# Optimization experiments

Measured on AMD Instinct MI355X. Metric: run time of the kernel, lower is better.

## Reference

```python
import jax, jax.numpy as jnp
import numpy as np

# Static configuration matching the selected code path:
#   mode='inject_subject', is_self_attn=True, layer_id='up_blocks.0' (inject layer, bank hit)
#   alpha = AlphaScheduler.alpha(step=20, total=50, 'up_blocks.0') = 0.8 * 0.6 = 0.48
B, L, D, H = 4, 1024, 1280, 20
DH = D // H  # 64
ALPHA = 0.48


def setup_inputs() -> dict:
    key = jax.random.key(0)
    ks = jax.random.split(key, 8)
    w = lambda k, shp: (jax.random.normal(k, shp, dtype=jnp.float32) * 0.02)
    return {
        "hidden_states": jax.random.normal(ks[0], (B, L, D), dtype=jnp.float32),
        "Wq": w(ks[1], (D, D)),
        "Wk": w(ks[2], (D, D)),
        "Wv": w(ks[3], (D, D)),
        "Wo": w(ks[4], (D, D)),
        "bo": jnp.zeros((D,), dtype=jnp.float32),
        # cached background K/V, stored after head_to_batch_dim -> [B*H, L_bg, DH]
        "K_bg": jax.random.normal(ks[5], (B * H, L, DH), dtype=jnp.float32),
        "V_bg": jax.random.normal(ks[6], (B * H, L, DH), dtype=jnp.float32),
    }


def _head_to_batch(x):  # [B, L, D] -> [B*H, L, DH]
    b, l, _ = x.shape
    return x.reshape(b, l, H, DH).transpose(0, 2, 1, 3).reshape(b * H, l, DH)


def _batch_to_head(x):  # [B*H, L, DH] -> [B, L, D]
    bh, l, _ = x.shape
    b = bh // H
    return x.reshape(b, H, l, DH).transpose(0, 2, 1, 3).reshape(b, l, D)


def reference(hidden_states, Wq, Wk, Wv, Wo, bo, K_bg, V_bg):
    # q/k/v projections (self-attention: k, v from hidden_states)
    q = _head_to_batch(hidden_states @ Wq)  # [B*H, L, DH]
    k = _head_to_batch(hidden_states @ Wk)
    v = _head_to_batch(hidden_states @ Wv)

    # inject_subject: concat cached background K/V scaled by alpha along kv-seq dim
    k = jnp.concatenate([k, ALPHA * K_bg], axis=1)  # [B*H, 2L, DH]
    v = jnp.concatenate([v, ALPHA * V_bg], axis=1)

    # _sdpa: q scaled by scale*sqrt(dh), SDPA divides by sqrt(dh) -> net factor `scale`
    scale = 1.0 / jnp.sqrt(jnp.asarray(DH, dtype=q.dtype))
    scores = jnp.einsum('bqd,bkd->bqk', q, k) * scale  # [B*H, L, 2L]
    probs = jax.nn.softmax(scores, axis=-1)
    context = jnp.einsum('bqk,bkd->bqd', probs, v)  # [B*H, L, DH]

    out = _batch_to_head(context) @ Wo + bo  # to_out[0] linear
    return out
```

## Files before the change

kernel.cpp:

```cpp
#include <hip/hip_runtime.h>
#include <hip/hip_bf16.h>

#define B_   4
#define L_   1024
#define D_   1280
#define H_   20
#define DH_  64
#define BH_  (B_*H_)
#define L2_  (2*L_)
#define ALPHA_ 0.48f
#define QSCALE_ 0.180336880f

typedef __attribute__((ext_vector_type(8))) short short8;
typedef __attribute__((ext_vector_type(4))) float float4v;

__device__ __forceinline__ float exp2_fast(float x) {
    float r;
    asm volatile("v_exp_f32 %0, %1" : "=v"(r) : "v"(x));
    return r;
}

__device__ __forceinline__ ushort f2bf(float f) {
    union { float f; unsigned int i; } v; v.f = f;
    unsigned int i = v.i;
    unsigned int r = i + 0x7FFF + ((i >> 16) & 1);
    return (ushort)(r >> 16);
}
__device__ __forceinline__ short8 pack8(float4 f0, float4 f1) {
    short8 o;
    o[0] = (short)f2bf(f0.x); o[1] = (short)f2bf(f0.y);
    o[2] = (short)f2bf(f0.z); o[3] = (short)f2bf(f0.w);
    o[4] = (short)f2bf(f1.x); o[5] = (short)f2bf(f1.y);
    o[6] = (short)f2bf(f1.z); o[7] = (short)f2bf(f1.w);
    return o;
}
__device__ __forceinline__ void pack4_store(ushort* dst, float a, float b, float c, float d) {
    union { __hip_bfloat162 h; unsigned int u; } x, y;
    x.h = __float22bfloat162_rn(make_float2(a, b));
    y.h = __float22bfloat162_rn(make_float2(c, d));
    uint2 v; v.x = x.u; v.y = y.u;
    *(uint2*)dst = v;
}

__device__ __forceinline__ void async16(const void* g, void* l) {
    __builtin_amdgcn_global_load_lds(
        (__attribute__((address_space(1))) void*)g,
        (__attribute__((address_space(3))) void*)l, 16, 0, 0);
}

__global__ __launch_bounds__(256) void prep(
    const float* __restrict__ w0, const float* __restrict__ w1,
    const float* __restrict__ w2, const float* __restrict__ w3,
    ushort* __restrict__ Wt,
    const float* __restrict__ Vbg, ushort* __restrict__ Vt,
    const float* __restrict__ X, ushort* __restrict__ Xb,
    const float* __restrict__ Kbg, ushort* __restrict__ Kcv) {
    int bi = blockIdx.x, tid = threadIdx.x;
    __shared__ __align__(16) ushort t[64 * 72];
    if (bi < 2880) {
        bool doScale = (bi >= 1600);
        const float* src; int srcld; long sbase;
        ushort* dst = nullptr; int dstld = 0; long dbase = 0;
        ushort* vout = nullptr;
        if (bi < 1600) {
            int z = bi / 400, t4 = bi % 400;
            int by = t4 / 20, bx = t4 % 20;
            const float* srcs[4] = {w0, w1, w2, w3};
            src = srcs[z]; srcld = D_; dstld = D_;
            sbase = (long)(by * 64) * D_ + bx * 64;
            dst = Wt + (long)z * D_ * D_;
            dbase = (long)(bx * 64) * D_ + by * 64;
        } else {
            int j = bi - 1600;
            int bh = j >> 4, kt = j & 15;
            src = Vbg; srcld = DH_;
            sbase = ((long)bh * L_ + kt * 64) * DH_;
            vout = Vt + (((long)bh * 32 + 16 + kt) << 12);
        }
        int ldr = tid >> 3, ldc = (tid & 7) * 8;
#pragma unroll
        for (int i = 0; i < 2; i++) {
            int y = ldr + 32 * i;
            long idx = sbase + (long)y * srcld + ldc;
            float4 f0 = *(const float4*)&src[idx];
            float4 f1 = *(const float4*)&src[idx + 4];
            if (doScale) {
                f0.x *= ALPHA_; f0.y *= ALPHA_; f0.z *= ALPHA_; f0.w *= ALPHA_;
                f1.x *= ALPHA_; f1.y *= ALPHA_; f1.z *= ALPHA_; f1.w *= ALPHA_;
            }
            *(short8*)&t[y * 72 + ldc] = pack8(f0, f1);
        }
        __syncthreads();
        if (bi < 1600) {
            int r8 = (tid & 7) * 8, c0 = tid >> 3;
#pragma unroll
            for (int i = 0; i < 2; i++) {
                int c = c0 + i * 32;
                short8 o;
#pragma unroll
                for (int j2 = 0; j2 < 8; j2++) o[j2] = (short)t[(r8 + j2) * 72 + c];
                *(short8*)&dst[dbase + (long)c * dstld + r8] = o;
            }
        } else {
#pragma unroll
            for (int i = 0; i < 2; i++) {
                int jj = i * 256 + tid;
                int cc = jj >> 6, d2 = jj & 63;
                short8 o;
#pragma unroll
                for (int e = 0; e < 8; e++) o[e] = (short)t[(cc * 8 + e) * 72 + d2];
                *(short8*)&vout[(long)jj * 8] = o;
            }
        }
    } else if (bi < 5440) {
        long i = ((long)(bi - 2880) * 256 + tid) * 8;
        *(short8*)&Xb[i] = pack8(*(const float4*)&X[i], *(const float4*)&X[i + 4]);
    } else {
        int j2 = bi - 5440;
        int bh = j2 >> 4, kt = j2 & 15;
        const float* src = Kbg + ((long)bh * L_ + kt * 64) * DH_;
#pragma unroll
        for (int i = 0; i < 2; i++) {
            int r = i * 256 + tid;
            int kv = r >> 3, cd = r & 7;
            long idx = (long)kv * 64 + cd * 8;
            *(short8*)&t[kv * 72 + cd * 8] =
                pack8(*(const float4*)&src[idx], *(const float4*)&src[idx + 4]);
        }
        __syncthreads();
        ushort* outp = Kcv + (((long)bh * 16 + kt) << 12);
#pragma unroll
        for (int i = 0; i < 2; i++) {
            int jj = i * 256 + tid;
            int c = jj >> 6, kv = jj & 63;
            *(short8*)&outp[(long)jj * 8] = *(const short8*)&t[kv * 72 + c * 8];
        }
    }
}

template<int BMt, int BNt, int WROWS, int WCOLS>
__global__ __launch_bounds__(256) void gemm_tpl(
    const ushort* __restrict__ A, const ushort* __restrict__ Bt,
    ushort* __restrict__ Qp, ushort* __restrict__ Kp, ushort* __restrict__ Vt,
    float* __restrict__ Out, const float* __restrict__ bo, int mode) {
    constexpr int MI = BMt / WROWS / 16;
    constexpr int NI = BNt / WCOLS / 16;
    constexpr int ASZ = BMt * 32, BSZ = BNt * 32;
    constexpr int RB = 1280 / BNt;
    __shared__ __align__(16) ushort Al[2 * ASZ];
    __shared__ __align__(16) ushort Bl[2 * BSZ];
    int tid = threadIdx.x;
    int bx = blockIdx.x, by = blockIdx.y;
    int w = tid >> 6, lane = tid & 63, l15 = lane & 15, quad = lane >> 4;
    int wm = (w / WCOLS) * (BMt / WROWS);
    int wn = (w % WCOLS) * (BNt / WCOLS);
    float4v acc[MI][NI] = {};
    const int K = 1280;
    constexpr int NK = 40;
    const ushort* Arow = A + (long)by * BMt * K + (tid >> 2) * K + (tid & 3) * 8;
    const ushort* Brow = Bt + (long)bx * BNt * K + (tid >> 2) * K + (tid & 3) * 8;

    auto stage = [&](int ki, int b) {
#pragma unroll
        for (int i = 0; i < BMt / 64; i++)
            async16(Arow + (long)i * 64 * K + ki * 32, &Al[b * ASZ + (i * 4 + w) * 512]);
#pragma unroll
        for (int i = 0; i < BNt / 64; i++)
            async16(Brow + (long)i * 64 * K + ki * 32, &Bl[b * BSZ + (i * 4 + w) * 512]);
    };

    stage(0, 0);
    __syncthreads();
    for (int ki = 0; ki < NK; ki++) {
        int cur = ki & 1;
        if (ki + 1 < NK) stage(ki + 1, 1 - cur);
        short8 av[MI], bv[NI];
#pragma unroll
        for (int mi = 0; mi < MI; mi++)
            av[mi] = *(const short8*)&Al[cur * ASZ + (wm + mi * 16 + l15) * 32 + quad * 8];
#pragma unroll
        for (int ni = 0; ni < NI; ni++)
            bv[ni] = *(const short8*)&Bl[cur * BSZ + (wn + ni * 16 + l15) * 32 + quad * 8];
#pragma unroll
        for (int mi = 0; mi < MI; mi++)
#pragma unroll
            for (int ni = 0; ni < NI; ni++)
                acc[mi][ni] = __builtin_amdgcn_mfma_f32_16x16x32_bf16(av[mi], bv[ni], acc[mi][ni], 0, 0, 0);
        __syncthreads();
    }

    if (mode == 0) {
        int which = bx / RB;
#pragma unroll
        for (int mi = 0; mi < MI; mi++) {
            int m0 = by * BMt + wm + mi * 16 + quad * 4;
            int b = m0 >> 10, l0 = m0 & 1023;
#pragma unroll
            for (int ni = 0; ni < NI; ni++) {
                int n = bx * BNt + wn + ni * 16 + l15;
                int np = n - which * 1280;
                int h = np >> 6, dh = np & 63;
                if (which == 0) {
#pragma unroll
                    for (int r = 0; r < 4; r++)
                        Qp[((long)(b * H_ + h) * L_ + l0 + r) * DH_ + dh] =
                            f2bf(acc[mi][ni][r] * QSCALE_);
                } else if (which == 1) {
                    long kb = ((((long)(b * H_ + h) * 16 + (l0 >> 6)) * 8 + (dh >> 3)) * 64
                               + (l0 & 63)) * 8 + (dh & 7);
#pragma unroll
                    for (int r = 0; r < 4; r++)
                        Kp[kb + r * 8] = f2bf(acc[mi][ni][r]);
                } else {
                    pack4_store(&Vt[((((long)(b * H_ + h) * 32 + (l0 >> 6)) * 8
                                      + ((l0 & 63) >> 3)) * 64 + dh) * 8 + (l0 & 7)],
                                acc[mi][ni][0], acc[mi][ni][1],
                                acc[mi][ni][2], acc[mi][ni][3]);
                }
            }
        }
    } else {
#pragma unroll
        for (int mi = 0; mi < MI; mi++) {
            int mloc = wm + mi * 16 + quad * 4;
#pragma unroll
            for (int ni = 0; ni < NI; ni++) {
                int nloc = wn + ni * 16 + l15;
#pragma unroll
                for (int r = 0; r < 4; r++) {
                    int m = by * BMt + mloc + r;
                    int n = bx * BNt + nloc;
                    Out[(long)m * D_ + n] = acc[mi][ni][r] + bo[n];
                }
            }
        }
    }
}

#define FS 72

__global__ __launch_bounds__(256) void flash_attn(
    const ushort* __restrict__ Qp, const ushort* __restrict__ Kp,
    const ushort* __restrict__ Kbg, const ushort* __restrict__ Vt,
    ushort* __restrict__ Ctx) {
    __shared__ __align__(16) ushort Kl[2 * 4096], Vl[2 * 4096];
    __shared__ __align__(16) ushort Pl[128 * FS];
    int tid = threadIdx.x;
    int w = tid >> 6, lane = tid & 63, l15 = lane & 15, quad = lane >> 4;
    int bi = blockIdx.x;
    int bh = (bi & 7) * 10 + ((bi >> 3) % 10);
    int qt = bi / 80;

    short8 aq[2][2];
    const ushort* Qb = Qp + ((long)bh * L_ + qt * 128 + w * 32) * DH_;
#pragma unroll
    for (int mi = 0; mi < 2; mi++)
#pragma unroll
        for (int ks = 0; ks < 2; ks++)
            aq[mi][ks] = *(const short8*)&Qb[(mi * 16 + l15) * DH_ + ks * 32 + quad * 8];

    float rs[2] = {0.f, 0.f};
    float4v O[2][4] = {};
    int prow = (w * 32 + l15) * FS;

    auto stage = [&](int kt, int b) {
        const ushort* Ksrc = (kt < 16)
            ? Kp  + (((long)bh * 16 + kt) << 12)
            : Kbg + (((long)bh * 16 + (kt - 16)) << 12);
        const ushort* Vsrc = Vt + (((long)bh * 32 + kt) << 12);
#pragma unroll
        for (int i = 0; i < 2; i++) {
            int c = w * 2 + i;
            async16(&Ksrc[c * 512 + lane * 8], &Kl[b * 4096 + c * 512]);
            async16(&Vsrc[c * 512 + lane * 8], &Vl[b * 4096 + c * 512]);
        }
    };

    stage(0, 0);
    __syncthreads();
    for (int kt = 0; kt < 32; kt++) {
        int cur = kt & 1;
        if (kt + 1 < 32) stage(kt + 1, 1 - cur);
        bool bg = (kt >= 16);
        float4v s[4][2] = {};
#pragma unroll
        for (int ks = 0; ks < 2; ks++) {
            short8 bk[4];
#pragma unroll
            for (int nt = 0; nt < 4; nt++)
                bk[nt] = *(const short8*)&Kl[cur * 4096 + (ks * 4 + quad) * 512 + (nt * 16 + l15) * 8];
#pragma unroll
            for (int nt = 0; nt < 4; nt++)
#pragma unroll
                for (int mi = 0; mi < 2; mi++)
                    s[nt][mi] = __builtin_amdgcn_mfma_f32_16x16x32_bf16(bk[nt], aq[mi][ks], s[nt][mi], 0, 0, 0);
        }
#pragma unroll
        for (int nt = 0; nt < 4; nt++)
#pragma unroll
            for (int mi = 0; mi < 2; mi++) {
                float p[4];
#pragma unroll
                for (int r = 0; r < 4; r++) {
                    float sv = s[nt][mi][r];
                    if (bg) sv *= ALPHA_;
                    p[r] = exp2_fast(sv);
                    rs[mi] += p[r];
                }
                pack4_store(&Pl[prow + mi * 16 * FS + nt * 16 + quad * 4],
                            p[0], p[1], p[2], p[3]);
            }
        asm volatile("s_waitcnt lgkmcnt(0)" ::: "memory");
        __builtin_amdgcn_sched_barrier(0);
#pragma unroll
        for (int ks = 0; ks < 2; ks++) {
            short8 bv[4];
#pragma unroll
            for (int nt = 0; nt < 4; nt++)
                bv[nt] = *(const short8*)&Vl[cur * 4096 + (ks * 4 + quad) * 512 + (nt * 16 + l15) * 8];
            short8 ap[2];
#pragma unroll
            for (int mi = 0; mi < 2; mi++)
                ap[mi] = *(const short8*)&Pl[prow + mi * 16 * FS + ks * 32 + quad * 8];
#pragma unroll
            for (int nt = 0; nt < 4; nt++)
#pragma unroll
                for (int mi = 0; mi < 2; mi++)
                    O[mi][nt] = __builtin_amdgcn_mfma_f32_16x16x32_bf16(bv[nt], ap[mi], O[mi][nt], 0, 0, 0);
        }
        __syncthreads();
    }
    int b = bh / H_, h = bh % H_;
#pragma unroll
    for (int mi = 0; mi < 2; mi++) {
        float v = rs[mi];
        v += __shfl_xor(v, 16);
        v += __shfl_xor(v, 32);
        float rcp = 1.f / v;
        long l = qt * 128 + w * 32 + mi * 16 + l15;
#pragma unroll
        for (int nt = 0; nt < 4; nt++)
            pack4_store(&Ctx[(long)(b * L_ + l) * D_ + h * DH_ + nt * 16 + quad * 4],
                        O[mi][nt][0] * rcp, O[mi][nt][1] * rcp,
                        O[mi][nt][2] * rcp, O[mi][nt][3] * rcp);
    }
}

extern "C" void kernel_launch(void* const* d_in, const int* in_sizes, int n_in,
                              void* d_out, int out_size, void* d_ws, size_t ws_size,
                              hipStream_t stream) {
    const float* X   = (const float*)d_in[0];
    const float* Wq  = (const float*)d_in[1];
    const float* Wk  = (const float*)d_in[2];
    const float* Wv  = (const float*)d_in[3];
    const float* Wo  = (const float*)d_in[4];
    const float* bo  = (const float*)d_in[5];
    const float* Kbg = (const float*)d_in[6];
    const float* Vbg = (const float*)d_in[7];

    char* ws = (char*)d_ws;
    size_t off = 0;
    auto alloc = [&](size_t bytes) {
        void* p = ws + off;
        off = (off + bytes + 255) & ~(size_t)255;
        return p;
    };
    ushort* Wt    = (ushort*)alloc((size_t)4 * D_ * D_ * 2);
    ushort* Qp    = (ushort*)alloc((size_t)BH_ * L_ * DH_ * 2);
    ushort* Kp    = (ushort*)alloc((size_t)BH_ * L_ * DH_ * 2);
    ushort* Kcv   = (ushort*)alloc((size_t)BH_ * L_ * DH_ * 2);
    ushort* Vt    = (ushort*)alloc((size_t)BH_ * DH_ * L2_ * 2);
    ushort* Xb    = (ushort*)alloc((size_t)B_ * L_ * D_ * 2);
    ushort* Ctx   = Xb;
    ushort* Wqkv_t = Wt;
    ushort* Wo_t   = Wt + (size_t)3 * D_ * D_;

    prep<<<6720, 256, 0, stream>>>(Wq, Wk, Wv, Wo, Wt, Vbg, Vt, X, Xb, Kbg, Kcv);
    gemm_tpl<128, 128, 2, 2><<<dim3(30, 32), 256, 0, stream>>>(
        Xb, Wqkv_t, Qp, Kp, Vt, nullptr, nullptr, 0);
    flash_attn<<<dim3(640), 256, 0, stream>>>(Qp, Kp, Kcv, Vt, Ctx);
    gemm_tpl<64, 128, 1, 4><<<dim3(10, 64), 256, 0, stream>>>(
        Ctx, Wo_t, nullptr, nullptr, nullptr, (float*)d_out, bo, 1);
}
```

Before: 309.2 us.

## Split attention KV range across two blocks and merge partials in combine kernel

The attention kernel now launches twice as many blocks. Each block handles either the self K/V half or the cached background half of the key sequence, and writes unnormalized fp32 partial outputs and row sums. A new combine kernel adds the two partials, normalizes by the summed row sums and writes bf16 context in head-interleaved layout. The aim is better load balance and CU occupancy during attention. The cost is an extra kernel launch and extra fp32 global traffic for the partial results.

```diff
diff --git a/kernel.cpp b/kernel.cpp
--- a/kernel.cpp
+++ b/kernel.cpp
@@ -242,14 +242,16 @@
 __global__ __launch_bounds__(256) void flash_attn(
     const ushort* __restrict__ Qp, const ushort* __restrict__ Kp,
     const ushort* __restrict__ Kbg, const ushort* __restrict__ Vt,
-    ushort* __restrict__ Ctx) {
+    float* __restrict__ Op, float* __restrict__ Rs) {
     __shared__ __align__(16) ushort Kl[2 * 4096], Vl[2 * 4096];
     __shared__ __align__(16) ushort Pl[128 * FS];
     int tid = threadIdx.x;
     int w = tid >> 6, lane = tid & 63, l15 = lane & 15, quad = lane >> 4;
     int bi = blockIdx.x;
-    int bh = (bi & 7) * 10 + ((bi >> 3) % 10);
-    int qt = bi / 80;
+    int s = bi >= 640; int ib = bi - s * 640;
+    int bh = (ib & 7) * 10 + ((ib >> 3) % 10);
+    int qt = ib / 80;
+    const int kt0 = s * 16;
 
     short8 aq[2][2];
     const ushort* Qb = Qp + ((long)bh * L_ + qt * 128 + w * 32) * DH_;
@@ -276,13 +278,13 @@
         }
     };
 
-    stage(0, 0);
+    stage(kt0, 0);
     __syncthreads();
-    for (int kt = 0; kt < 32; kt++) {
+    for (int kt = kt0; kt < kt0 + 16; kt++) {
         int cur = kt & 1;
-        if (kt + 1 < 32) stage(kt + 1, 1 - cur);
+        if (kt + 1 < kt0 + 16) stage(kt + 1, 1 - cur);
         bool bg = (kt >= 16);
-        float4v s[4][2] = {};
+        float4v s4[4][2] = {};
 #pragma unroll
         for (int ks = 0; ks < 2; ks++) {
             short8 bk[4];
@@ -293,7 +295,7 @@
             for (int nt = 0; nt < 4; nt++)
 #pragma unroll
                 for (int mi = 0; mi < 2; mi++)
-                    s[nt][mi] = __builtin_amdgcn_mfma_f32_16x16x32_bf16(bk[nt], aq[mi][ks], s[nt][mi], 0, 0, 0);
+                    s4[nt][mi] = __builtin_amdgcn_mfma_f32_16x16x32_bf16(bk[nt], aq[mi][ks], s4[nt][mi], 0, 0, 0);
         }
 #pragma unroll
         for (int nt = 0; nt < 4; nt++)
@@ -302,7 +304,7 @@
                 float p[4];
 #pragma unroll
                 for (int r = 0; r < 4; r++) {
-                    float sv = s[nt][mi][r];
+                    float sv = s4[nt][mi][r];
                     if (bg) sv *= ALPHA_;
                     p[r] = exp2_fast(sv);
                     rs[mi] += p[r];
@@ -330,20 +332,38 @@
         }
         __syncthreads();
     }
-    int b = bh / H_, h = bh % H_;
 #pragma unroll
     for (int mi = 0; mi < 2; mi++) {
         float v = rs[mi];
         v += __shfl_xor(v, 16);
         v += __shfl_xor(v, 32);
-        float rcp = 1.f / v;
         long l = qt * 128 + w * 32 + mi * 16 + l15;
+        long row = ((long)s * BH_ + bh) * L_ + l;
 #pragma unroll
         for (int nt = 0; nt < 4; nt++)
-            pack4_store(&Ctx[(long)(b * L_ + l) * D_ + h * DH_ + nt * 16 + quad * 4],
-                        O[mi][nt][0] * rcp, O[mi][nt][1] * rcp,
-                        O[mi][nt][2] * rcp, O[mi][nt][3] * rcp);
+            *(float4v*)&Op[row * DH_ + nt * 16 + quad * 4] = O[mi][nt];
+        if (quad == 0) Rs[row] = v;
     }
+}
+
+__global__ __launch_bounds__(256) void combine(
+    const float* __restrict__ Op, const float* __restrict__ Rs,
+    ushort* __restrict__ Ctx) {
+    long idx = (long)blockIdx.x * 256 + threadIdx.x;
+    long row = idx >> 3;
+    int d0 = ((int)idx & 7) * 8;
+    long bh = row >> 10, l = row & 1023;
+    const float* p0 = Op + row * DH_ + d0;
+    const float* p1 = Op + ((long)BH_ * L_ + row) * DH_ + d0;
+    float rcp = 1.f / (Rs[row] + Rs[(long)BH_ * L_ + row]);
+    float4 a0 = *(const float4*)p0, a1 = *(const float4*)(p0 + 4);
+    float4 b0 = *(const float4*)p1, b1 = *(const float4*)(p1 + 4);
+    float4 c0 = make_float4((a0.x + b0.x) * rcp, (a0.y + b0.y) * rcp,
+                            (a0.z + b0.z) * rcp, (a0.w + b0.w) * rcp);
+    float4 c1 = make_float4((a1.x + b1.x) * rcp, (a1.y + b1.y) * rcp,
+                            (a1.z + b1.z) * rcp, (a1.w + b1.w) * rcp);
+    long b = bh / H_, h = bh % H_;
+    *(short8*)&Ctx[((b * L_ + l) * D_) + h * DH_ + d0] = pack8(c0, c1);
 }
 
 extern "C" void kernel_launch(void* const* d_in, const int* in_sizes, int n_in,
@@ -371,6 +391,8 @@
     ushort* Kcv   = (ushort*)alloc((size_t)BH_ * L_ * DH_ * 2);
     ushort* Vt    = (ushort*)alloc((size_t)BH_ * DH_ * L2_ * 2);
     ushort* Xb    = (ushort*)alloc((size_t)B_ * L_ * D_ * 2);
+    float*  Opar  = (float*)alloc((size_t)2 * BH_ * L_ * DH_ * 4);
+    float*  Rspar = (float*)alloc((size_t)2 * BH_ * L_ * 4);
     ushort* Ctx   = Xb;
     ushort* Wqkv_t = Wt;
     ushort* Wo_t   = Wt + (size_t)3 * D_ * D_;
@@ -378,7 +400,8 @@
     prep<<<6720, 256, 0, stream>>>(Wq, Wk, Wv, Wo, Wt, Vbg, Vt, X, Xb, Kbg, Kcv);
     gemm_tpl<128, 128, 2, 2><<<dim3(30, 32), 256, 0, stream>>>(
         Xb, Wqkv_t, Qp, Kp, Vt, nullptr, nullptr, 0);
-    flash_attn<<<dim3(640), 256, 0, stream>>>(Qp, Kp, Kcv, Vt, Ctx);
+    flash_attn<<<dim3(1280), 256, 0, stream>>>(Qp, Kp, Kcv, Vt, Opar, Rspar);
+    combine<<<dim3(2560), 256, 0, stream>>>(Opar, Rspar, Ctx);
     gemm_tpl<64, 128, 1, 4><<<dim3(10, 64), 256, 0, stream>>>(
         Ctx, Wo_t, nullptr, nullptr, nullptr, (float*)d_out, bo, 1);
 }
```

Result: no change. 312.4 us (+1.0%).

## Keep softmax probabilities in registers by permuting V layout to match MFMA output

Applied to the files above, without the earlier changes.

The flash attention kernel no longer writes the exponentiated scores to a shared-memory P buffer and reads them back. The probabilities are packed straight from the QK^T MFMA accumulators into the A operand of the PV MFMA. To keep this correct, the V transpose layout written by both the projection GEMM epilogue and the background-V preprocessing is permuted along the key dimension so it matches the accumulator row order. This removes LDS traffic, an lgkmcnt wait and LDS footprint per tile, but depends on getting the index permutation exactly right in three places.

```diff
diff --git a/kernel.cpp b/kernel.cpp
--- a/kernel.cpp
+++ b/kernel.cpp
@@ -106,9 +106,11 @@
             for (int i = 0; i < 2; i++) {
                 int jj = i * 256 + tid;
                 int cc = jj >> 6, d2 = jj & 63;
+                int rb = (cc >> 2) * 32 + (cc & 3) * 4;
                 short8 o;
 #pragma unroll
-                for (int e = 0; e < 8; e++) o[e] = (short)t[(cc * 8 + e) * 72 + d2];
+                for (int e = 0; e < 8; e++)
+                    o[e] = (short)t[(rb + (e >> 2) * 16 + (e & 3)) * 72 + d2];
                 *(short8*)&vout[(long)jj * 8] = o;
             }
         }
@@ -212,8 +214,11 @@
                     for (int r = 0; r < 4; r++)
                         Kp[kb + r * 8] = f2bf(acc[mi][ni][r]);
                 } else {
+                    int j = l0 & 63;
+                    int cc = ((j >> 5) << 2) | ((j >> 2) & 3);
+                    int eb = ((j >> 4) & 1) << 2;
                     pack4_store(&Vt[((((long)(b * H_ + h) * 32 + (l0 >> 6)) * 8
-                                      + ((l0 & 63) >> 3)) * 64 + dh) * 8 + (l0 & 7)],
+                                      + cc) * 64 + dh) * 8 + eb],
                                 acc[mi][ni][0], acc[mi][ni][1],
                                 acc[mi][ni][2], acc[mi][ni][3]);
                 }
@@ -237,14 +242,11 @@
     }
 }
 
-#define FS 72
-
 __global__ __launch_bounds__(256) void flash_attn(
     const ushort* __restrict__ Qp, const ushort* __restrict__ Kp,
     const ushort* __restrict__ Kbg, const ushort* __restrict__ Vt,
     ushort* __restrict__ Ctx) {
     __shared__ __align__(16) ushort Kl[2 * 4096], Vl[2 * 4096];
-    __shared__ __align__(16) ushort Pl[128 * FS];
     int tid = threadIdx.x;
     int w = tid >> 6, lane = tid & 63, l15 = lane & 15, quad = lane >> 4;
     int bi = blockIdx.x;
@@ -261,7 +263,6 @@
 
     float rs[2] = {0.f, 0.f};
     float4v O[2][4] = {};
-    int prow = (w * 32 + l15) * FS;
 
     auto stage = [&](int kt, int b) {
         const ushort* Ksrc = (kt < 16)
@@ -282,7 +283,7 @@
         int cur = kt & 1;
         if (kt + 1 < 32) stage(kt + 1, 1 - cur);
         bool bg = (kt >= 16);
-        float4v s[4][2] = {};
+        float4v s4[4][2] = {};
 #pragma unroll
         for (int ks = 0; ks < 2; ks++) {
             short8 bk[4];
@@ -293,40 +294,41 @@
             for (int nt = 0; nt < 4; nt++)
 #pragma unroll
                 for (int mi = 0; mi < 2; mi++)
-                    s[nt][mi] = __builtin_amdgcn_mfma_f32_16x16x32_bf16(bk[nt], aq[mi][ks], s[nt][mi], 0, 0, 0);
-        }
-#pragma unroll
-        for (int nt = 0; nt < 4; nt++)
-#pragma unroll
-            for (int mi = 0; mi < 2; mi++) {
-                float p[4];
+                    s4[nt][mi] = __builtin_amdgcn_mfma_f32_16x16x32_bf16(bk[nt], aq[mi][ks], s4[nt][mi], 0, 0, 0);
+        }
+        short8 ap[2][2];
+#pragma unroll
+        for (int mi = 0; mi < 2; mi++) {
+            float p[4][4];
+#pragma unroll
+            for (int nt = 0; nt < 4; nt++)
 #pragma unroll
                 for (int r = 0; r < 4; r++) {
-                    float sv = s[nt][mi][r];
+                    float sv = s4[nt][mi][r];
                     if (bg) sv *= ALPHA_;
-                    p[r] = exp2_fast(sv);
-                    rs[mi] += p[r];
+                    p[nt][r] = exp2_fast(sv);
+                    rs[mi] += p[nt][r];
                 }
-                pack4_store(&Pl[prow + mi * 16 * FS + nt * 16 + quad * 4],
-                            p[0], p[1], p[2], p[3]);
-            }
-        asm volatile("s_waitcnt lgkmcnt(0)" ::: "memory");
-        __builtin_amdgcn_sched_barrier(0);
+#pragma unroll
+            for (int ks = 0; ks < 2; ks++) {
+                float4 f0 = make_float4(p[2 * ks][0], p[2 * ks][1],
+                                        p[2 * ks][2], p[2 * ks][3]);
+                float4 f1 = make_float4(p[2 * ks + 1][0], p[2 * ks + 1][1],
+                                        p[2 * ks + 1][2], p[2 * ks + 1][3]);
+                ap[mi][ks] = pack8(f0, f1);
+            }
+        }
 #pragma unroll
         for (int ks = 0; ks < 2; ks++) {
             short8 bv[4];
 #pragma unroll
             for (int nt = 0; nt < 4; nt++)
                 bv[nt] = *(const short8*)&Vl[cur * 4096 + (ks * 4 + quad) * 512 + (nt * 16 + l15) * 8];
-            short8 ap[2];
-#pragma unroll
-            for (int mi = 0; mi < 2; mi++)
-                ap[mi] = *(const short8*)&Pl[prow + mi * 16 * FS + ks * 32 + quad * 8];
 #pragma unroll
             for (int nt = 0; nt < 4; nt++)
 #pragma unroll
                 for (int mi = 0; mi < 2; mi++)
-                    O[mi][nt] = __builtin_amdgcn_mfma_f32_16x16x32_bf16(bv[nt], ap[mi], O[mi][nt], 0, 0, 0);
+                    O[mi][nt] = __builtin_amdgcn_mfma_f32_16x16x32_bf16(bv[nt], ap[mi][ks], O[mi][nt], 0, 0, 0);
         }
         __syncthreads();
     }
```

Measured after the change: 310.0 us. About the same (+0.3%).
